# Performance work log

Hardware: AMD Instinct MI355X
Metric: run time of the kernel (lower is better)

The kernel has to match this reference:

```python
import jax, jax.numpy as jnp
import numpy as np

B, S, D, H = 4, 2048, 1024, 16
HD = D // H

def setup_inputs() -> dict:
    key = jax.random.key(0)
    k1, k2, k3 = jax.random.split(key, 3)
    x = jax.random.normal(k1, (B, S, D), dtype=jnp.float32)
    W_qkv = jax.random.normal(k2, (D, 3 * D), dtype=jnp.float32) * (1.0 / np.sqrt(D))
    W_out = jax.random.normal(k3, (D, D), dtype=jnp.float32) * (1.0 / np.sqrt(D))
    causal_mask = jnp.tril(jnp.ones((S, S), dtype=bool))[None, None]  # [1,1,S,S]
    return {"x": x, "causal_mask": causal_mask, "W_qkv": W_qkv, "W_out": W_out}

def reference(x, causal_mask, W_qkv, W_out):
    b, s, d = x.shape
    scale = 1.0 / np.sqrt(HD)
    qkv = x @ W_qkv  # [b,s,3d]
    q, k, v = jnp.split(qkv, 3, axis=-1)
    # [b,h,s,hd]
    q = q.reshape(b, s, H, HD).transpose(0, 2, 1, 3)
    k = k.reshape(b, s, H, HD).transpose(0, 2, 1, 3)
    v = v.reshape(b, s, H, HD).transpose(0, 2, 1, 3)
    scores = jnp.einsum('bhqd,bhkd->bhqk', q, k) * scale
    scores = jnp.where(causal_mask, scores, -jnp.inf)
    attn = jax.nn.softmax(scores, axis=-1)
    out = jnp.einsum('bhqk,bhkd->bhqd', attn, v)
    out = out.transpose(0, 2, 1, 3).reshape(b, s, d)
    return out @ W_out
```

## Files before the change

kernel.cpp:

```cpp
#include <hip/hip_runtime.h>
#include <hip/hip_bf16.h>

typedef __bf16 bf16;
typedef unsigned short u16;
typedef unsigned int u32;
typedef __attribute__((ext_vector_type(8))) __bf16 bf16x8;
typedef __attribute__((ext_vector_type(4))) unsigned short u16x4;
typedef __attribute__((ext_vector_type(4))) float f32x4;

#define B_  4
#define S_  2048
#define D_  1024
#define H_  16
#define HD_ 64

#define QSCALE 0.18033688f

__device__ inline u16 bf16_bits(float f) {
  bf16 h = (bf16)f;
  return __builtin_bit_cast(u16, h);
}

__device__ __forceinline__ void glds16(const bf16* g, bf16* s) {
  __builtin_amdgcn_global_load_lds(
      (const __attribute__((address_space(1))) void*)g,
      (__attribute__((address_space(3))) void*)s, 16, 0, 0);
}

#define MEMFENCE() asm volatile("" ::: "memory")
#define BARRIER_RAW() __builtin_amdgcn_s_barrier()
#define LGKM0() asm volatile("s_waitcnt lgkmcnt(0)" ::: "memory")
#define VMCNT(n) asm volatile("s_waitcnt vmcnt(" #n ")" ::: "memory")

__global__ void cvt_x(const float* __restrict__ in, bf16* __restrict__ out, long n) {
  long i = ((long)blockIdx.x * 256 + threadIdx.x) * 8;
  if (i < n) {
    f32x4 a = *(const f32x4*)(in + i);
    f32x4 b = *(const f32x4*)(in + i + 4);
    bf16x8 v;
#pragma unroll
    for (int j = 0; j < 4; ++j) { v[j] = (bf16)a[j]; v[4 + j] = (bf16)b[j]; }
    *(bf16x8*)(out + i) = v;
  }
}

__global__ void cvt_w(const float* __restrict__ in, bf16* __restrict__ out,
                      int K, int N) {
  __shared__ float tile[32][33];
  int n0 = blockIdx.x * 32, k0 = blockIdx.y * 32;
  int x = threadIdx.x, y = threadIdx.y;
#pragma unroll
  for (int i = 0; i < 32; i += 8)
    tile[y + i][x] = in[(long)(k0 + y + i) * N + (n0 + x)];
  __syncthreads();
#pragma unroll
  for (int i = 0; i < 32; i += 8)
    out[(long)(n0 + y + i) * K + (k0 + x)] = (bf16)tile[x][y + i];
}

template <typename TC>
__launch_bounds__(256)
__global__ void gemm128(const bf16* __restrict__ A, const bf16* __restrict__ Bt,
                        TC* __restrict__ C, int M, int N, int K) {
  __shared__ __attribute__((aligned(16))) bf16 As[8][512];
  __shared__ __attribute__((aligned(16))) bf16 Bs[8][512];
  int t = threadIdx.x;
  int w = t >> 6, lane = t & 63;
  int wr = w >> 1, wc = w & 1;
  int fr = lane & 15, fq = lane >> 4;
  long m0 = (long)blockIdx.y * 128, n0 = (long)blockIdx.x * 128;
  f32x4 acc[4][4] = {};
  const bf16* ag = A  + (m0 + (2 * w) * 16 + fr) * (long)K + fq * 8;
  const bf16* bg = Bt + (n0 + (2 * w) * 16 + fr) * (long)K + fq * 8;
  bf16* al0 = &As[2 * w][0];
  bf16* al1 = &As[2 * w + 1][0];
  bf16* bl0 = &Bs[2 * w][0];
  bf16* bl1 = &Bs[2 * w + 1][0];
  const long K16 = 16 * (long)K;
  for (int k0 = 0; k0 < K; k0 += 32) {
    __syncthreads();
    glds16(ag + k0, al0);
    glds16(ag + k0 + K16, al1);
    glds16(bg + k0, bl0);
    glds16(bg + k0 + K16, bl1);
    __syncthreads();
    bf16x8 af[4], bfv[4];
#pragma unroll
    for (int i = 0; i < 4; ++i) {
      af[i]  = *(const bf16x8*)&As[wr * 4 + i][lane * 8];
      bfv[i] = *(const bf16x8*)&Bs[wc * 4 + i][lane * 8];
    }
#pragma unroll
    for (int mb = 0; mb < 4; ++mb)
#pragma unroll
      for (int nb = 0; nb < 4; ++nb)
        acc[mb][nb] = __builtin_amdgcn_mfma_f32_16x16x32_bf16(
            af[mb], bfv[nb], acc[mb][nb], 0, 0, 0);
  }
#pragma unroll
  for (int mb = 0; mb < 4; ++mb) {
    long row = m0 + wr * 64 + mb * 16 + fq * 4;
#pragma unroll
    for (int nb = 0; nb < 4; ++nb) {
      long col = n0 + wc * 64 + nb * 16 + fr;
#pragma unroll
      for (int i = 0; i < 4; ++i)
        C[(row + i) * (long)N + col] = (TC)acc[mb][nb][i];
    }
  }
}

#define QUAD(HM, HN)                                                          \
  do {                                                                        \
    _Pragma("unroll") for (int m2 = 0; m2 < 4; ++m2) {                        \
      _Pragma("unroll") for (int n2 = 0; n2 < 2; ++n2) {                      \
        _Pragma("unroll") for (int kc = 0; kc < 2; ++kc)                      \
            acc[(HM) * 4 + m2][(HN) * 2 + n2] =                               \
                __builtin_amdgcn_mfma_f32_16x16x32_bf16(                      \
                    aF[m2][kc], bF[(HN) * 2 + n2][kc],                        \
                    acc[(HM) * 4 + m2][(HN) * 2 + n2], 0, 0, 0);              \
      }                                                                       \
    }                                                                         \
  } while (0)

__launch_bounds__(512, 2)
__global__ void gemm_qkv(const bf16* __restrict__ A, const bf16* __restrict__ Bt,
                         bf16* __restrict__ qk, bf16* __restrict__ vT) {
  __shared__ __attribute__((aligned(16))) bf16 smem[2][4][8192];
  const int K = 1024;
  int t = threadIdx.x;
  int w = t >> 6, lane = t & 63;
  int wm = w >> 2, wn = w & 3;
  int fr = lane & 15, fq = lane >> 4;
  long m0 = (long)blockIdx.y * 256, n0 = (long)blockIdx.x * 256;

  int o = t * 16;
  int p = o ^ (((o >> 9) & 1) << 5);
  int si = p >> 10;
  int srow = (si >> 1) * 16 + ((p & 1023) >> 6);
  int scol = (si & 1) * 32 + ((p & 63) >> 1);
  const bf16* aS = A  + (m0 + srow) * (long)K + scol;
  const bf16* bS = Bt + (n0 + srow) * (long)K + scol;

  int fro = (fr << 6) + (fq << 4);
  fro ^= (fr & 8) << 2;
  const char* Afr0 = (const char*)&smem[0][wm][0] + fro;
  const char* Bfr0 = (const char*)&smem[0][2 + (wn >> 1)][0] + ((wn & 1) << 13) + fro;
  bf16* s00 = &smem[0][0][0];

  f32x4 acc[8][4] = {};
  bf16x8 aF[4][2], bF[4][2];

#define STAGE(src, dstRegion)                          \
  do {                                                 \
    glds16((src), (dstRegion) + w * 512);              \
    glds16((src) + 65536, (dstRegion) + 4096 + w * 512); \
  } while (0)

  STAGE(aS,               s00);
  STAGE(aS + 131072,      s00 + 8192);
  STAGE(bS,               s00 + 16384);
  STAGE(bS + 131072,      s00 + 24576);
  STAGE(bS + 64,          s00 + 32768 + 16384);
  STAGE(bS + 64 + 131072, s00 + 32768 + 24576);
  VMCNT(4);
  MEMFENCE(); BARRIER_RAW(); MEMFENCE();

  for (int j = 0; j < 16; ++j) {
    int b = j & 1, nb = b ^ 1;
    long kA = (long)((j + 1 < 16) ? j + 1 : 15) * 64;
    long kB = (long)((j + 2 < 16) ? j + 2 : 15) * 64;
    const char* Ab = Afr0 + b * 65536;
    const char* Bb = Bfr0 + b * 65536;
    bf16* sA0 = s00 + nb * 32768;
    bf16* sB0 = s00 + b * 32768 + 16384;

#pragma unroll
    for (int m2 = 0; m2 < 4; ++m2)
#pragma unroll
      for (int kc = 0; kc < 2; ++kc)
        aF[m2][kc] = *(const bf16x8*)(Ab + (m2 * 2 + kc) * 1024);
#pragma unroll
    for (int n2 = 0; n2 < 2; ++n2)
#pragma unroll
      for (int kc = 0; kc < 2; ++kc)
        bF[n2][kc] = *(const bf16x8*)(Bb + (n2 * 2 + kc) * 1024);
    STAGE(aS + kA, sA0);
    MEMFENCE(); BARRIER_RAW(); LGKM0();
    __builtin_amdgcn_s_setprio(1);
    QUAD(0, 0);
    __builtin_amdgcn_s_setprio(0);
    MEMFENCE(); BARRIER_RAW(); MEMFENCE();

#pragma unroll
    for (int n2 = 2; n2 < 4; ++n2)
#pragma unroll
      for (int kc = 0; kc < 2; ++kc)
        bF[n2][kc] = *(const bf16x8*)(Bb + (n2 * 2 + kc) * 1024);
    STAGE(aS + kA + 131072, sA0 + 8192);
    MEMFENCE(); BARRIER_RAW(); LGKM0();
    __builtin_amdgcn_s_setprio(1);
    QUAD(0, 1);
    __builtin_amdgcn_s_setprio(0);
    MEMFENCE(); BARRIER_RAW(); MEMFENCE();

#pragma unroll
    for (int m2 = 0; m2 < 4; ++m2)
#pragma unroll
      for (int kc = 0; kc < 2; ++kc)
        aF[m2][kc] = *(const bf16x8*)(Ab + ((4 + m2) * 2 + kc) * 1024);
    STAGE(bS + kB, sB0);
    MEMFENCE(); BARRIER_RAW(); LGKM0();
    __builtin_amdgcn_s_setprio(1);
    QUAD(1, 1);
    __builtin_amdgcn_s_setprio(0);
    MEMFENCE(); BARRIER_RAW(); MEMFENCE();

    STAGE(bS + kB + 131072, sB0 + 8192);
    MEMFENCE(); BARRIER_RAW(); LGKM0();
    __builtin_amdgcn_s_setprio(1);
    QUAD(1, 0);
    __builtin_amdgcn_s_setprio(0);
    VMCNT(4);
    MEMFENCE(); BARRIER_RAW(); MEMFENCE();
  }
#undef STAGE

#pragma unroll
  for (int fm = 0; fm < 8; ++fm) {
    long row = m0 + wm * 128 + fm * 16 + fq * 4;
    long bb = row >> 11;
    long s0 = row & 2047;
#pragma unroll
    for (int fn = 0; fn < 4; ++fn) {
      long col = n0 + wn * 64 + fn * 16 + fr;
      if (col < 2048) {
        float sc = (col < 1024) ? QSCALE : 1.f;
#pragma unroll
        for (int i = 0; i < 4; ++i)
          qk[(row + i) * 2048 + col] = (bf16)(acc[fm][fn][i] * sc);
      } else {
        u16x4 pk;
#pragma unroll
        for (int i = 0; i < 4; ++i) pk[i] = bf16_bits(acc[fm][fn][i]);
        *(u16x4*)(vT + (bb * 1024 + (col - 2048)) * 2048 + s0) = pk;
      }
    }
  }
}

__launch_bounds__(256, 3)
__global__ void attn_mfma3(const bf16* __restrict__ qk, const bf16* __restrict__ vT,
                           bf16* __restrict__ out) {
  __shared__ __attribute__((aligned(16))) bf16 Ks[2][4][2][512];
  __shared__ __attribute__((aligned(16))) bf16 Vs[2][4][2][512];
  __shared__ __attribute__((aligned(16))) bf16 Pb[4][16][76];
  int bx = blockIdx.x;
  int st = 15 - (bx >> 6);
  int hb = bx & 63;
  int h = hb >> 2, b = hb & 3;
  int t = threadIdx.x, w = t >> 6, lane = t & 63;
  int fr = lane & 15, fq = lane >> 4;
  const bf16* qkb = qk + (long)b * S_ * 2048;
  const bf16* vTb = vT + ((long)b * 1024 + h * HD_) * 2048;
  bf16* ob = out + (long)b * S_ * D_ + h * HD_;

  bf16x8 ones;
#pragma unroll
  for (int j = 0; j < 8; ++j) ones[j] = (bf16)1.0f;

  const bf16* kg0 = qkb + (long)(w * 16 + fr) * 2048 + 1024 + h * HD_ + fq * 8;
  const bf16* vg0 = vTb + (long)(w * 16 + fr) * 2048 + fq * 8;

  int qbase = st * 128 + w * 32;
  int jtmax = 2 * st + 1;

  glds16(kg0,      &Ks[0][w][0][0]);
  glds16(kg0 + 32, &Ks[0][w][1][0]);
  glds16(vg0,      &Vs[0][w][0][0]);
  glds16(vg0 + 32, &Vs[0][w][1][0]);

  bf16x8 aQ[2][2];
#pragma unroll
  for (int s = 0; s < 2; ++s)
#pragma unroll
    for (int kc = 0; kc < 2; ++kc)
      aQ[s][kc] = *(const bf16x8*)(qkb + (long)(qbase + s * 16 + fr) * 2048 +
                                   h * HD_ + kc * 32 + fq * 8);
  f32x4 acc_o[2][4] = {};
  f32x4 acc_l[2] = {};

  for (int jt = 0; jt <= jtmax; ++jt) {
    int c = jt & 1;
    __syncthreads();
    if (jt < jtmax) {
      int n = c ^ 1;
      const bf16* kg = kg0 + (long)(jt + 1) * 64 * 2048;
      const bf16* vg = vg0 + (jt + 1) * 64;
      glds16(kg,      &Ks[n][w][0][0]);
      glds16(kg + 32, &Ks[n][w][1][0]);
      glds16(vg,      &Vs[n][w][0][0]);
      glds16(vg + 32, &Vs[n][w][1][0]);
    }
    bf16x8 bK[4][2], bV[4][2];
#pragma unroll
    for (int nb = 0; nb < 4; ++nb)
#pragma unroll
      for (int kc = 0; kc < 2; ++kc) {
        bK[nb][kc] = *(const bf16x8*)&Ks[c][nb][kc][lane * 8];
        bV[nb][kc] = *(const bf16x8*)&Vs[c][nb][kc][lane * 8];
      }
#pragma unroll
    for (int s = 0; s < 2; ++s) {
      int dlim = qbase + s * 16 - jt * 64;
      if (dlim <= -16) continue;
      f32x4 acc_s[4] = {};
      __builtin_amdgcn_s_setprio(1);
#pragma unroll
      for (int nb = 0; nb < 4; ++nb) {
        acc_s[nb] = __builtin_amdgcn_mfma_f32_16x16x32_bf16(aQ[s][0], bK[nb][0], acc_s[nb], 0, 0, 0);
        acc_s[nb] = __builtin_amdgcn_mfma_f32_16x16x32_bf16(aQ[s][1], bK[nb][1], acc_s[nb], 0, 0, 0);
      }
      __builtin_amdgcn_s_setprio(0);
      if (dlim < 63) {
#pragma unroll
        for (int i = 0; i < 4; ++i) {
          int qa = dlim + fq * 4 + i;
#pragma unroll
          for (int nb = 0; nb < 4; ++nb) {
            float pv = exp2f(acc_s[nb][i]);
            if (nb * 16 + fr > qa) pv = 0.f;
            Pb[w][fq * 4 + i][nb * 16 + fr] = (bf16)pv;
          }
        }
      } else {
#pragma unroll
        for (int i = 0; i < 4; ++i)
#pragma unroll
          for (int nb = 0; nb < 4; ++nb) {
            float pv = exp2f(acc_s[nb][i]);
            Pb[w][fq * 4 + i][nb * 16 + fr] = (bf16)pv;
          }
      }
      __builtin_amdgcn_s_setprio(1);
#pragma unroll
      for (int kc = 0; kc < 2; ++kc) {
        bf16x8 aP = *(const bf16x8*)&Pb[w][fr][kc * 32 + fq * 8];
        acc_l[s] = __builtin_amdgcn_mfma_f32_16x16x32_bf16(aP, ones, acc_l[s], 0, 0, 0);
#pragma unroll
        for (int nb = 0; nb < 4; ++nb)
          acc_o[s][nb] = __builtin_amdgcn_mfma_f32_16x16x32_bf16(aP, bV[nb][kc], acc_o[s][nb], 0, 0, 0);
      }
      __builtin_amdgcn_s_setprio(0);
    }
  }
#pragma unroll
  for (int s = 0; s < 2; ++s) {
    long r0 = (long)(qbase + s * 16 + fq * 4);
#pragma unroll
    for (int i = 0; i < 4; ++i) {
      float inv = 1.f / acc_l[s][i];
#pragma unroll
      for (int nb = 0; nb < 4; ++nb)
        ob[(r0 + i) * D_ + nb * 16 + fr] = (bf16)(acc_o[s][nb][i] * inv);
    }
  }
}

__global__ void sentinel_k(float* out, float v, int n) {
  int i = blockIdx.x * 256 + threadIdx.x;
  if (i < n) out[i] = v;
}

extern "C" void kernel_launch(void* const* d_in, const int* in_sizes, int n_in,
                              void* d_out, int out_size, void* d_ws, size_t ws_size,
                              hipStream_t stream) {
  const float* x    = (const float*)d_in[0];
  const float* Wqkv = (const float*)d_in[2];
  const float* Wout = (const float*)d_in[3];
  float* out = (float*)d_out;

  const size_t SD = (size_t)S_ * D_;
  bf16* qk     = (bf16*)d_ws;
  bf16* vT     = qk + (size_t)8192 * 2048;
  bf16* x_bf   = vT + (size_t)4 * 1024 * 2048;
  bf16* ao     = x_bf;
  bf16* wqkv_t = x_bf + (size_t)8192 * 1024;
  bf16* wout_t = wqkv_t + (size_t)3072 * 1024;
  size_t need = ((size_t)16777216 + 8388608 + 8388608 + 3145728 + 1048576) * sizeof(bf16);

  if (ws_size >= need) {
    cvt_x<<<4096, 256, 0, stream>>>(x, x_bf, (long)(B_ * SD));
    cvt_w<<<dim3(3072 / 32, 1024 / 32), dim3(32, 8), 0, stream>>>(Wqkv, wqkv_t, 1024, 3072);
    cvt_w<<<dim3(1024 / 32, 1024 / 32), dim3(32, 8), 0, stream>>>(Wout, wout_t, 1024, 1024);
    gemm_qkv<<<dim3(3072 / 256, (B_ * S_) / 256), 512, 0, stream>>>(
        x_bf, wqkv_t, qk, vT);
    attn_mfma3<<<dim3(1024, 1, 1), 256, 0, stream>>>(qk, vT, ao);
    gemm128<float><<<dim3(D_ / 128, (B_ * S_) / 128), 256, 0, stream>>>(
        ao, wout_t, out, B_ * S_, D_, D_);
  } else {
    float v = 1000.f + (float)(ws_size >> 20);
    int n = (int)((size_t)B_ * SD);
    sentinel_k<<<(n + 255) / 256, 256, 0, stream>>>(out, v, n);
  }
}
```

Measured before the change: 281.1 us.

## Keep softmax probabilities in registers via transposed MFMA and permuted K rows

Swaps the MFMA operand order so the score tile comes out transposed (keys along the register dimension), and permutes the K rows loaded into LDS so each lane's accumulator values line up with the B-operand layout of the PV MFMA. The probabilities are packed directly into bf16x8 registers instead of going through an LDS round-trip buffer, and the output is stored as packed 4-element vectors. This removes the LDS writes and reads of P and the shared buffer, at the cost of a trickier index mapping for the causal mask and row sums.

```diff
diff --git a/kernel.cpp b/kernel.cpp
--- a/kernel.cpp
+++ b/kernel.cpp
@@ -254,7 +254,6 @@
                            bf16* __restrict__ out) {
   __shared__ __attribute__((aligned(16))) bf16 Ks[2][4][2][512];
   __shared__ __attribute__((aligned(16))) bf16 Vs[2][4][2][512];
-  __shared__ __attribute__((aligned(16))) bf16 Pb[4][16][76];
   int bx = blockIdx.x;
   int st = 15 - (bx >> 6);
   int hb = bx & 63;
@@ -269,7 +268,8 @@
 #pragma unroll
   for (int j = 0; j < 8; ++j) ones[j] = (bf16)1.0f;
 
-  const bf16* kg0 = qkb + (long)(w * 16 + fr) * 2048 + 1024 + h * HD_ + fq * 8;
+  int kappa = 8 * (fr >> 2) + (fr & 3) + 4 * (w & 1) + 32 * (w >> 1);
+  const bf16* kg0 = qkb + (long)kappa * 2048 + 1024 + h * HD_ + fq * 8;
   const bf16* vg0 = vTb + (long)(w * 16 + fr) * 2048 + fq * 8;
 
   int qbase = st * 128 + w * 32;
@@ -318,51 +318,56 @@
       __builtin_amdgcn_s_setprio(1);
 #pragma unroll
       for (int nb = 0; nb < 4; ++nb) {
-        acc_s[nb] = __builtin_amdgcn_mfma_f32_16x16x32_bf16(aQ[s][0], bK[nb][0], acc_s[nb], 0, 0, 0);
-        acc_s[nb] = __builtin_amdgcn_mfma_f32_16x16x32_bf16(aQ[s][1], bK[nb][1], acc_s[nb], 0, 0, 0);
+        acc_s[nb] = __builtin_amdgcn_mfma_f32_16x16x32_bf16(bK[nb][0], aQ[s][0], acc_s[nb], 0, 0, 0);
+        acc_s[nb] = __builtin_amdgcn_mfma_f32_16x16x32_bf16(bK[nb][1], aQ[s][1], acc_s[nb], 0, 0, 0);
       }
       __builtin_amdgcn_s_setprio(0);
+      float pe[4][4];
       if (dlim < 63) {
-#pragma unroll
-        for (int i = 0; i < 4; ++i) {
-          int qa = dlim + fq * 4 + i;
-#pragma unroll
-          for (int nb = 0; nb < 4; ++nb) {
+        int kbase = 8 * fq;
+        int qoff = dlim + fr;
+#pragma unroll
+        for (int nb = 0; nb < 4; ++nb) {
+          int ko = kbase + 4 * (nb & 1) + 32 * (nb >> 1);
+#pragma unroll
+          for (int i = 0; i < 4; ++i) {
             float pv = exp2f(acc_s[nb][i]);
-            if (nb * 16 + fr > qa) pv = 0.f;
-            Pb[w][fq * 4 + i][nb * 16 + fr] = (bf16)pv;
+            pe[nb][i] = (ko + i > qoff) ? 0.f : pv;
           }
         }
       } else {
 #pragma unroll
-        for (int i = 0; i < 4; ++i)
-#pragma unroll
-          for (int nb = 0; nb < 4; ++nb) {
-            float pv = exp2f(acc_s[nb][i]);
-            Pb[w][fq * 4 + i][nb * 16 + fr] = (bf16)pv;
-          }
+        for (int nb = 0; nb < 4; ++nb)
+#pragma unroll
+          for (int i = 0; i < 4; ++i) pe[nb][i] = exp2f(acc_s[nb][i]);
       }
+      bf16x8 pf[2];
+#pragma unroll
+      for (int kc = 0; kc < 2; ++kc)
+#pragma unroll
+        for (int e = 0; e < 8; ++e)
+          pf[kc][e] = (bf16)pe[2 * kc + (e >> 2)][e & 3];
       __builtin_amdgcn_s_setprio(1);
 #pragma unroll
       for (int kc = 0; kc < 2; ++kc) {
-        bf16x8 aP = *(const bf16x8*)&Pb[w][fr][kc * 32 + fq * 8];
-        acc_l[s] = __builtin_amdgcn_mfma_f32_16x16x32_bf16(aP, ones, acc_l[s], 0, 0, 0);
+        acc_l[s] = __builtin_amdgcn_mfma_f32_16x16x32_bf16(ones, pf[kc], acc_l[s], 0, 0, 0);
 #pragma unroll
         for (int nb = 0; nb < 4; ++nb)
-          acc_o[s][nb] = __builtin_amdgcn_mfma_f32_16x16x32_bf16(aP, bV[nb][kc], acc_o[s][nb], 0, 0, 0);
+          acc_o[s][nb] = __builtin_amdgcn_mfma_f32_16x16x32_bf16(bV[nb][kc], pf[kc], acc_o[s][nb], 0, 0, 0);
       }
       __builtin_amdgcn_s_setprio(0);
     }
   }
 #pragma unroll
   for (int s = 0; s < 2; ++s) {
-    long r0 = (long)(qbase + s * 16 + fq * 4);
-#pragma unroll
-    for (int i = 0; i < 4; ++i) {
-      float inv = 1.f / acc_l[s][i];
-#pragma unroll
-      for (int nb = 0; nb < 4; ++nb)
-        ob[(r0 + i) * D_ + nb * 16 + fr] = (bf16)(acc_o[s][nb][i] * inv);
+    float inv = 1.f / acc_l[s][0];
+    long q = (long)(qbase + s * 16 + fr);
+#pragma unroll
+    for (int nb = 0; nb < 4; ++nb) {
+      u16x4 pk;
+#pragma unroll
+      for (int i = 0; i < 4; ++i) pk[i] = bf16_bits(acc_o[s][nb][i] * inv);
+      *(u16x4*)(ob + q * D_ + nb * 16 + fq * 4) = pk;
     }
   }
 }
```

Result: faster. 271.8 us (-3.3%).
